# Performance work log

Hardware: AMD Instinct MI355X
Metric: run time of the kernel (lower is better)

## Reference

```python
import jax, jax.numpy as jnp
import numpy as np

TOTAL_SEQ = 32768
NUM_HEADS = 16
HEAD_DIM = 80
WINDOW = 64
NUM_WINDOWS = TOTAL_SEQ // WINDOW


def setup_inputs() -> dict:
    key = jax.random.key(0)
    kq, kk, kv, ka = jax.random.split(key, 4)
    q = jax.random.normal(kq, (TOTAL_SEQ, NUM_HEADS, HEAD_DIM), dtype=jnp.float32)
    k = jax.random.normal(kk, (TOTAL_SEQ, NUM_HEADS, HEAD_DIM), dtype=jnp.float32)
    v = jax.random.normal(kv, (TOTAL_SEQ, NUM_HEADS, HEAD_DIM), dtype=jnp.float32)
    # realistic rope tables: cos/sin of random angles (mimics 2D vision rope output)
    angles = jax.random.uniform(ka, (TOTAL_SEQ, HEAD_DIM // 2), dtype=jnp.float32) * (2.0 * np.pi)
    cos = jnp.cos(angles)
    sin = jnp.sin(angles)
    # uniform windows of size WINDOW, as produced by Qwen-VL window partitioning
    cu_seqlens = (jnp.arange(NUM_WINDOWS + 1, dtype=jnp.int32) * WINDOW)
    return {"q": q, "k": k, "v": v, "cos": cos, "sin": sin, "cu_seqlens": cu_seqlens}


def reference(q, k, v, cos, sin, cu_seqlens):
    # q,k,v: [S, H, D]; cos,sin: [S, D//2]; cu_seqlens: [num_windows+1], uniform windows
    S, H, D = q.shape
    nw = cu_seqlens.shape[0] - 1
    W = S // nw  # window length (static)
    half = D // 2

    c = cos[:, None, :]  # [S, 1, half]
    s = sin[:, None, :]

    def rope(x):
        # pairwise rotation between first/second halves, exactly as the kernel does
        x0, x1 = x[..., :half], x[..., half:]
        return jnp.concatenate([x0 * c - x1 * s, x0 * s + x1 * c], axis=-1)

    qr = rope(q).reshape(nw, W, H, D)
    kr = rope(k).reshape(nw, W, H, D)
    vw = v.reshape(nw, W, H, D)

    scale = 1.0 / jnp.sqrt(jnp.asarray(D, dtype=jnp.float32))
    scores = jnp.einsum('nqhd,nkhd->nhqk', qr, kr) * scale  # [nw, H, W, W]
    p = jax.nn.softmax(scores.astype(jnp.float32), axis=-1).astype(v.dtype)
    out = jnp.einsum('nhqk,nkhd->nqhd', p, vw)  # [nw, W, H, D]
    return out.reshape(S, H, D)
```

## Files before the change

kernel.cpp:

```cpp
#include <hip/hip_runtime.h>

typedef __attribute__((ext_vector_type(8))) short short8;
typedef __attribute__((ext_vector_type(4))) float f32x4;

#define NH 16
#define HD 80
#define SH (NH*HD)
#define WIN 64

__device__ __forceinline__ unsigned short f2bf(float x) {
    union { float f; unsigned int u; } c; c.f = x;
    unsigned int u = c.u;
    u = (u + 0x7FFFu + ((u >> 16) & 1u)) >> 16;
    return (unsigned short)u;
}
__device__ __forceinline__ float bf2f(unsigned short h) {
    union { unsigned int u; float f; } c; c.u = ((unsigned int)h) << 16;
    return c.f;
}

__global__ __launch_bounds__(256, 2) void win_attn(
    const float* __restrict__ q, const float* __restrict__ k,
    const float* __restrict__ v, const float* __restrict__ cosb,
    const float* __restrict__ sinb, float* __restrict__ out)
{
    __shared__ unsigned short Qh[64*104];
    __shared__ unsigned short Ql[64*104];
    __shared__ unsigned short Kh[64*104];
    __shared__ unsigned short Kl[64*104];
    __shared__ unsigned short Vt[80*72];
    __shared__ unsigned short Ps[64*72];

    const int head = blockIdx.x & (NH - 1);
    const int win  = blockIdx.x >> 4;
    const int tid  = threadIdx.x;
    const int tok0 = win * WIN;

    for (int idx = tid; idx < 640; idx += 256) {
        const int row = idx / 10;
        const int c0  = (idx % 10) * 4;
        const size_t goff = (size_t)(tok0 + row) * SH + head * HD + c0;
        const float4 qa = *(const float4*)(q + goff);
        const float4 qb = *(const float4*)(q + goff + 40);
        const float4 ka = *(const float4*)(k + goff);
        const float4 kb = *(const float4*)(k + goff + 40);
        const size_t coff = (size_t)(tok0 + row) * 40 + c0;
        const float4 cc = *(const float4*)(cosb + coff);
        const float4 ss = *(const float4*)(sinb + coff);
        const int o0 = row * 104 + c0;
        #pragma unroll
        for (int i = 0; i < 4; ++i) {
            const float ci = ((const float*)&cc)[i], si = ((const float*)&ss)[i];
            const float q0 = ((const float*)&qa)[i], q1 = ((const float*)&qb)[i];
            const float k0 = ((const float*)&ka)[i], k1 = ((const float*)&kb)[i];
            const float qr0 = q0 * ci - q1 * si, qr1 = q0 * si + q1 * ci;
            const float kr0 = k0 * ci - k1 * si, kr1 = k0 * si + k1 * ci;
            unsigned short h;
            h = f2bf(qr0); Qh[o0 + i]      = h; Ql[o0 + i]      = f2bf(qr0 - bf2f(h));
            h = f2bf(qr1); Qh[o0 + 40 + i] = h; Ql[o0 + 40 + i] = f2bf(qr1 - bf2f(h));
            h = f2bf(kr0); Kh[o0 + i]      = h; Kl[o0 + i]      = f2bf(kr0 - bf2f(h));
            h = f2bf(kr1); Kh[o0 + 40 + i] = h; Kl[o0 + 40 + i] = f2bf(kr1 - bf2f(h));
        }
    }
    for (int idx = tid; idx < 1024; idx += 256) {
        const int o = (idx >> 4) * 104 + 80 + (idx & 15);
        Qh[o] = 0; Ql[o] = 0; Kh[o] = 0; Kl[o] = 0;
    }
    for (int idx = tid; idx < 1280; idx += 256) {
        const int row = idx / 20;
        const int c   = (idx % 20) * 4;
        const float4 vv = *(const float4*)(v + (size_t)(tok0 + row) * SH + head * HD + c);
        Vt[(c + 0) * 72 + row] = f2bf(vv.x);
        Vt[(c + 1) * 72 + row] = f2bf(vv.y);
        Vt[(c + 2) * 72 + row] = f2bf(vv.z);
        Vt[(c + 3) * 72 + row] = f2bf(vv.w);
    }
    __syncthreads();

    const int wave = tid >> 6;
    const int lane = tid & 63;
    const int l15  = lane & 15;
    const int lg   = lane >> 4;

    f32x4 accS[4] = {{0,0,0,0},{0,0,0,0},{0,0,0,0},{0,0,0,0}};
    const int arow = (wave * 16 + l15) * 104;
    #pragma unroll
    for (int st = 0; st < 3; ++st) {
        const int ko = st * 32 + lg * 8;
        const short8 ah = *(const short8*)&Qh[arow + ko];
        const short8 al = *(const short8*)&Ql[arow + ko];
        #pragma unroll
        for (int t = 0; t < 4; ++t) {
            const int brow = (t * 16 + l15) * 104 + ko;
            const short8 bh = *(const short8*)&Kh[brow];
            const short8 bl = *(const short8*)&Kl[brow];
            accS[t] = __builtin_amdgcn_mfma_f32_16x16x32_bf16(ah, bh, accS[t], 0, 0, 0);
            accS[t] = __builtin_amdgcn_mfma_f32_16x16x32_bf16(ah, bl, accS[t], 0, 0, 0);
            accS[t] = __builtin_amdgcn_mfma_f32_16x16x32_bf16(al, bh, accS[t], 0, 0, 0);
        }
    }

    const float scale = 0.11180339887498949f;
    #pragma unroll
    for (int reg = 0; reg < 4; ++reg) {
        float m = fmaxf(fmaxf(accS[0][reg], accS[1][reg]),
                        fmaxf(accS[2][reg], accS[3][reg]));
        #pragma unroll
        for (int msk = 8; msk; msk >>= 1) m = fmaxf(m, __shfl_xor(m, msk));
        float p[4]; float sum = 0.f;
        #pragma unroll
        for (int t = 0; t < 4; ++t) { p[t] = __expf((accS[t][reg] - m) * scale); sum += p[t]; }
        #pragma unroll
        for (int msk = 8; msk; msk >>= 1) sum += __shfl_xor(sum, msk);
        const float inv = 1.f / sum;
        const int prow = (wave * 16 + lg * 4 + reg) * 72;
        #pragma unroll
        for (int t = 0; t < 4; ++t) Ps[prow + t * 16 + l15] = f2bf(p[t] * inv);
    }
    __syncthreads();

    f32x4 accO[5] = {{0,0,0,0},{0,0,0,0},{0,0,0,0},{0,0,0,0},{0,0,0,0}};
    const int parow = (wave * 16 + l15) * 72;
    #pragma unroll
    for (int st = 0; st < 2; ++st) {
        const int ko = st * 32 + lg * 8;
        const short8 pf = *(const short8*)&Ps[parow + ko];
        #pragma unroll
        for (int t = 0; t < 5; ++t) {
            const short8 vf = *(const short8*)&Vt[(t * 16 + l15) * 72 + ko];
            accO[t] = __builtin_amdgcn_mfma_f32_16x16x32_bf16(pf, vf, accO[t], 0, 0, 0);
        }
    }

    const int orow = tok0 + wave * 16 + lg * 4;
    #pragma unroll
    for (int t = 0; t < 5; ++t) {
        #pragma unroll
        for (int r = 0; r < 4; ++r) {
            out[(size_t)(orow + r) * SH + head * HD + t * 16 + l15] = accO[t][r];
        }
    }
}

extern "C" void kernel_launch(void* const* d_in, const int* in_sizes, int n_in,
                              void* d_out, int out_size, void* d_ws, size_t ws_size,
                              hipStream_t stream) {
    const float* q    = (const float*)d_in[0];
    const float* k    = (const float*)d_in[1];
    const float* v    = (const float*)d_in[2];
    const float* cosb = (const float*)d_in[3];
    const float* sinb = (const float*)d_in[4];
    float* out = (float*)d_out;
    win_attn<<<dim3(8192), dim3(256), 0, stream>>>(q, k, v, cosb, sinb, out);
}
```

Baseline: 528.7 us.

## Drop Q low-part MFMA, alias shared buffers, prefetch V into registers

Removes the Q low-order bf16 split, so QK^T uses two MFMAs per tile instead of three. Shared memory is cut from about 64KB to about 40KB by aliasing P onto Q and Vt onto Kl, with an extra barrier, and launch bounds are raised to 4 blocks per CU. V is loaded into registers at kernel start and written to LDS after the score phase, overlapping its global latency with compute. Q is now rounded to bf16, which lowers score precision, and the 20 extra registers for V may pressure occupancy.

```diff
diff --git a/kernel.cpp b/kernel.cpp
--- a/kernel.cpp
+++ b/kernel.cpp
@@ -19,22 +19,31 @@
     return c.f;
 }
 
-__global__ __launch_bounds__(256, 2) void win_attn(
+__global__ __launch_bounds__(256, 4) void win_attn(
     const float* __restrict__ q, const float* __restrict__ k,
     const float* __restrict__ v, const float* __restrict__ cosb,
     const float* __restrict__ sinb, float* __restrict__ out)
 {
-    __shared__ unsigned short Qh[64*104];
-    __shared__ unsigned short Ql[64*104];
-    __shared__ unsigned short Kh[64*104];
-    __shared__ unsigned short Kl[64*104];
-    __shared__ unsigned short Vt[80*72];
-    __shared__ unsigned short Ps[64*72];
+    __shared__ unsigned short sm[19968];
+    unsigned short* const Qh = sm;
+    unsigned short* const Kh = sm + 6656;
+    unsigned short* const Kl = sm + 13312;
+    unsigned short* const Ps = sm;
+    unsigned short* const Vt = sm + 13312;
 
     const int head = blockIdx.x & (NH - 1);
     const int win  = blockIdx.x >> 4;
     const int tid  = threadIdx.x;
     const int tok0 = win * WIN;
+
+    float4 vreg[5];
+    #pragma unroll
+    for (int j = 0; j < 5; ++j) {
+        const int idx = tid + 256 * j;
+        const int row = idx / 20;
+        const int c   = (idx % 20) * 4;
+        vreg[j] = *(const float4*)(v + (size_t)(tok0 + row) * SH + head * HD + c);
+    }
 
     for (int idx = tid; idx < 640; idx += 256) {
         const int row = idx / 10;
@@ -55,25 +64,16 @@
             const float k0 = ((const float*)&ka)[i], k1 = ((const float*)&kb)[i];
             const float qr0 = q0 * ci - q1 * si, qr1 = q0 * si + q1 * ci;
             const float kr0 = k0 * ci - k1 * si, kr1 = k0 * si + k1 * ci;
+            Qh[o0 + i]      = f2bf(qr0);
+            Qh[o0 + 40 + i] = f2bf(qr1);
             unsigned short h;
-            h = f2bf(qr0); Qh[o0 + i]      = h; Ql[o0 + i]      = f2bf(qr0 - bf2f(h));
-            h = f2bf(qr1); Qh[o0 + 40 + i] = h; Ql[o0 + 40 + i] = f2bf(qr1 - bf2f(h));
             h = f2bf(kr0); Kh[o0 + i]      = h; Kl[o0 + i]      = f2bf(kr0 - bf2f(h));
             h = f2bf(kr1); Kh[o0 + 40 + i] = h; Kl[o0 + 40 + i] = f2bf(kr1 - bf2f(h));
         }
     }
     for (int idx = tid; idx < 1024; idx += 256) {
         const int o = (idx >> 4) * 104 + 80 + (idx & 15);
-        Qh[o] = 0; Ql[o] = 0; Kh[o] = 0; Kl[o] = 0;
-    }
-    for (int idx = tid; idx < 1280; idx += 256) {
-        const int row = idx / 20;
-        const int c   = (idx % 20) * 4;
-        const float4 vv = *(const float4*)(v + (size_t)(tok0 + row) * SH + head * HD + c);
-        Vt[(c + 0) * 72 + row] = f2bf(vv.x);
-        Vt[(c + 1) * 72 + row] = f2bf(vv.y);
-        Vt[(c + 2) * 72 + row] = f2bf(vv.z);
-        Vt[(c + 3) * 72 + row] = f2bf(vv.w);
+        Qh[o] = 0; Kh[o] = 0; Kl[o] = 0;
     }
     __syncthreads();
 
@@ -88,7 +88,6 @@
     for (int st = 0; st < 3; ++st) {
         const int ko = st * 32 + lg * 8;
         const short8 ah = *(const short8*)&Qh[arow + ko];
-        const short8 al = *(const short8*)&Ql[arow + ko];
         #pragma unroll
         for (int t = 0; t < 4; ++t) {
             const int brow = (t * 16 + l15) * 104 + ko;
@@ -96,8 +95,19 @@
             const short8 bl = *(const short8*)&Kl[brow];
             accS[t] = __builtin_amdgcn_mfma_f32_16x16x32_bf16(ah, bh, accS[t], 0, 0, 0);
             accS[t] = __builtin_amdgcn_mfma_f32_16x16x32_bf16(ah, bl, accS[t], 0, 0, 0);
-            accS[t] = __builtin_amdgcn_mfma_f32_16x16x32_bf16(al, bh, accS[t], 0, 0, 0);
         }
+    }
+    __syncthreads();
+
+    #pragma unroll
+    for (int j = 0; j < 5; ++j) {
+        const int idx = tid + 256 * j;
+        const int row = idx / 20;
+        const int c   = (idx % 20) * 4;
+        Vt[(c + 0) * 72 + row] = f2bf(vreg[j].x);
+        Vt[(c + 1) * 72 + row] = f2bf(vreg[j].y);
+        Vt[(c + 2) * 72 + row] = f2bf(vreg[j].z);
+        Vt[(c + 3) * 72 + row] = f2bf(vreg[j].w);
     }
 
     const float scale = 0.11180339887498949f;
```

After: 498.7 us. 1.06x faster.
